# Optimization experiments

Measured on AMD Instinct MI355X. Metric: run time of the kernel, lower is better.

Reference implementation:

```python
import jax, jax.numpy as jnp
import numpy as np

H = 1024      # hidden_size
NH = 16       # num heads
HD = H // NH  # head dim


def setup_inputs() -> dict:
    key = jax.random.key(0)
    ks = jax.random.split(key, 10)
    s = 1.0 / np.sqrt(H)
    return {
        "hidden_states": jax.random.normal(ks[0], (2, 2048, H), jnp.float32),
        "attention_mask": jnp.zeros((2, 1, 1, 2048), jnp.float32),
        "Wq": jax.random.uniform(ks[1], (H, H), jnp.float32, -s, s),
        "bq": jnp.zeros((H,), jnp.float32),
        "Wk": jax.random.uniform(ks[2], (H, H), jnp.float32, -s, s),
        "bk": jnp.zeros((H,), jnp.float32),
        "Wv": jax.random.uniform(ks[3], (H, H), jnp.float32, -s, s),
        "bv": jnp.zeros((H,), jnp.float32),
        "Wo": jax.random.uniform(ks[4], (H, H), jnp.float32, -s, s),
        "bo": jnp.zeros((H,), jnp.float32),
    }


def _split_heads(x):
    b, s, _ = x.shape
    return x.reshape(b, s, NH, HD).transpose(0, 2, 1, 3)  # [B,NH,S,HD]


def reference(hidden_states, attention_mask, Wq, bq, Wk, bk, Wv, bv, Wo, bo):
    q = _split_heads(hidden_states @ Wq.T + bq)
    k = _split_heads(hidden_states @ Wk.T + bk)
    v = _split_heads(hidden_states @ Wv.T + bv)
    scores = jnp.einsum("bhqd,bhkd->bhqk", q, k) / np.sqrt(HD)
    scores = scores + attention_mask
    probs = jax.nn.softmax(scores, axis=-1)  # dropout prob=0 / eval mode -> no-op
    ctx = jnp.einsum("bhqk,bhkd->bhqd", probs, v)
    b, _, s, _ = ctx.shape
    ctx = ctx.transpose(0, 2, 1, 3).reshape(b, s, H)
    return ctx @ Wo.T + bo
```

## Files before the change

kernel.cpp:

```cpp
#include <hip/hip_runtime.h>
#include <hip/hip_bf16.h>

typedef __bf16 bf16_t;
typedef __bf16 bf16x8 __attribute__((ext_vector_type(8)));
typedef float f32x4 __attribute__((ext_vector_type(4)));
typedef float f32x16 __attribute__((ext_vector_type(16)));
typedef unsigned short u16;

#define DEVI __device__ __forceinline__
#define MFMA16x16x32(A, B, C) __builtin_amdgcn_mfma_f32_16x16x32_bf16(A, B, C, 0, 0, 0)
#define MFMA32x32x16(A, B, C) __builtin_amdgcn_mfma_f32_32x32x16_bf16(A, B, C, 0, 0, 0)

DEVI void gload_lds16(const void* g, void* l) {
  __builtin_amdgcn_global_load_lds(
      (const __attribute__((address_space(1))) void*)g,
      (__attribute__((address_space(3))) void*)l, 16, 0, 0);
}

DEVI u16 bits_of(bf16_t x) { return __builtin_bit_cast(u16, x); }

DEVI unsigned pk2(float lo, float hi) {
  return (unsigned)bits_of((bf16_t)lo) | ((unsigned)bits_of((bf16_t)hi) << 16);
}

DEVI bf16x8 mk_frag(unsigned s0, unsigned s1, unsigned s2, unsigned s3) {
  int4 t;
  t.x = (int)s0; t.y = (int)s1; t.z = (int)s2; t.w = (int)s3;
  return __builtin_bit_cast(bf16x8, t);
}

#if __has_builtin(__builtin_amdgcn_exp2f)
DEVI float exp2_fast(float x) { return __builtin_amdgcn_exp2f(x); }
#else
DEVI float exp2_fast(float x) { return __exp2f(x); }
#endif

__global__ void cvt_all(const float4* __restrict__ X,
                        const float4* __restrict__ Wq, const float4* __restrict__ Wk,
                        const float4* __restrict__ Wv, const float4* __restrict__ Wo,
                        ushort4* __restrict__ out) {
  int i = blockIdx.x * 256 + threadIdx.x;
  const float4* src;
  int off;
  if (i < 1048576) { src = X; off = i; }
  else {
    int j = i - 1048576;
    int seg = j >> 18;
    off = j & 262143;
    src = (seg == 0) ? Wq : (seg == 1) ? Wk : (seg == 2) ? Wv : Wo;
  }
  float4 v = src[off];
  ushort4 o;
  o.x = bits_of((bf16_t)v.x);
  o.y = bits_of((bf16_t)v.y);
  o.z = bits_of((bf16_t)v.z);
  o.w = bits_of((bf16_t)v.w);
  out[i] = o;
}

__global__ __launch_bounds__(256, 3) void gemm_bt(
    const bf16_t* __restrict__ A,
    const bf16_t* __restrict__ W0, const bf16_t* __restrict__ W1, const bf16_t* __restrict__ W2,
    const float* __restrict__ b0, const float* __restrict__ b1, const float* __restrict__ b2,
    bf16_t* o0, bf16_t* o1, bf16_t* o2, float s0, float s1, float s2) {
  constexpr int K = 1024, N = 1024;
  const int z = blockIdx.z;
  const bf16_t* W = (z == 0) ? W0 : ((z == 1) ? W1 : W2);
  const float* bias = (z == 0) ? b0 : ((z == 1) ? b1 : b2);
  bf16_t* out = (z == 0) ? o0 : ((z == 1) ? o1 : o2);
  const float scale = (z == 0) ? s0 : ((z == 1) ? s1 : s2);

  __shared__ bf16_t As[128 * 32];
  __shared__ bf16_t Bs[128 * 32];

  const int tid = threadIdx.x;
  const int wave = tid >> 6, lane = tid & 63;
  const int g = lane >> 4, l15 = lane & 15;
  const long m0 = (long)blockIdx.x * 128;
  const long n0 = (long)blockIdx.y * 128;

  const int srow = lane >> 2;
  const int scol = (lane & 3) * 8;

  const int wr = (wave >> 1) * 64;
  const int wc = (wave & 1) * 64;

  f32x4 acc[4][4] = {};

  for (int k0 = 0; k0 < K; k0 += 32) {
    __syncthreads();
#pragma unroll
    for (int t = 0; t < 2; ++t) {
      int chunk = wave * 2 + t;
      int row = chunk * 16 + srow;
      gload_lds16(A + (m0 + row) * K + k0 + scol, (char*)As + chunk * 1024);
      gload_lds16(W + (n0 + row) * K + k0 + scol, (char*)Bs + chunk * 1024);
    }
    __syncthreads();

    bf16x8 af[4], bfr[4];
#pragma unroll
    for (int i = 0; i < 4; ++i)
      af[i] = *(const bf16x8*)(As + (wr + i * 16 + l15) * 32 + g * 8);
#pragma unroll
    for (int i = 0; i < 4; ++i)
      bfr[i] = *(const bf16x8*)(Bs + (wc + i * 16 + l15) * 32 + g * 8);
    __builtin_amdgcn_s_setprio(1);
#pragma unroll
    for (int mi = 0; mi < 4; ++mi)
#pragma unroll
      for (int ni = 0; ni < 4; ++ni)
        acc[mi][ni] = MFMA16x16x32(af[mi], bfr[ni], acc[mi][ni]);
    __builtin_amdgcn_s_setprio(0);
  }

#pragma unroll
  for (int ni = 0; ni < 4; ++ni) {
    long col = n0 + wc + ni * 16 + l15;
    float bv = bias[col];
#pragma unroll
    for (int mi = 0; mi < 4; ++mi) {
#pragma unroll
      for (int r = 0; r < 4; ++r) {
        long row = m0 + wr + mi * 16 + g * 4 + r;
        out[row * N + col] = (bf16_t)((acc[mi][ni][r] + bv) * scale);
      }
    }
  }
}

__global__ __launch_bounds__(256, 3) void gemm_o64(
    const bf16_t* __restrict__ A, const bf16_t* __restrict__ W,
    const float* __restrict__ bias, float* __restrict__ out) {
  constexpr int K = 1024, N = 1024;
  __shared__ bf16_t As[128 * 32];
  __shared__ bf16_t Bs[64 * 32];

  const int tid = threadIdx.x;
  const int wave = tid >> 6, lane = tid & 63;
  const int g = lane >> 4, l15 = lane & 15;
  const long m0 = (long)blockIdx.x * 128;
  const long n0 = (long)blockIdx.y * 64;

  const int srow = lane >> 2;
  const int scol = (lane & 3) * 8;

  const int wr = (wave >> 1) * 64;
  const int wc = (wave & 1) * 32;

  f32x4 acc[4][2] = {};

  for (int k0 = 0; k0 < K; k0 += 32) {
    __syncthreads();
#pragma unroll
    for (int c = 0; c < 3; ++c) {
      int idx = wave * 3 + c;
      if (idx < 8) {
        int row = idx * 16 + srow;
        gload_lds16(A + (m0 + row) * K + k0 + scol, (char*)As + idx * 1024);
      } else {
        int row = (idx - 8) * 16 + srow;
        gload_lds16(W + (n0 + row) * K + k0 + scol, (char*)Bs + (idx - 8) * 1024);
      }
    }
    __syncthreads();

    bf16x8 af[4], bfr[2];
#pragma unroll
    for (int i = 0; i < 4; ++i)
      af[i] = *(const bf16x8*)(As + (wr + i * 16 + l15) * 32 + g * 8);
#pragma unroll
    for (int i = 0; i < 2; ++i)
      bfr[i] = *(const bf16x8*)(Bs + (wc + i * 16 + l15) * 32 + g * 8);
    __builtin_amdgcn_s_setprio(1);
#pragma unroll
    for (int mi = 0; mi < 4; ++mi)
#pragma unroll
      for (int ni = 0; ni < 2; ++ni)
        acc[mi][ni] = MFMA16x16x32(af[mi], bfr[ni], acc[mi][ni]);
    __builtin_amdgcn_s_setprio(0);
  }

#pragma unroll
  for (int ni = 0; ni < 2; ++ni) {
    long col = n0 + wc + ni * 16 + l15;
    float bv = bias[col];
#pragma unroll
    for (int mi = 0; mi < 4; ++mi) {
#pragma unroll
      for (int r = 0; r < 4; ++r) {
        long row = m0 + wr + mi * 16 + g * 4 + r;
        out[row * N + col] = acc[mi][ni][r] + bv;
      }
    }
  }
}

__global__ __launch_bounds__(256, 2) void attn_fwd10(
    const bf16_t* __restrict__ Qm, const bf16_t* __restrict__ Km,
    const bf16_t* __restrict__ Vm, const float* __restrict__ mask,
    bf16_t* __restrict__ ctx) {
  constexpr int S = 2048, Hs = 1024;
  constexpr float L2E = 1.4426950408889634f;
  int id = blockIdx.y * 16 + blockIdx.x;
  int swz = ((id & 7) << 6) | (id >> 3);
  const int qb = swz & 15;
  const int bh = swz >> 4;
  const int b = bh >> 4, h = bh & 15;

  const int tid = threadIdx.x;
  const int wave = tid >> 6, lane = tid & 63;
  const int l31 = lane & 31, hi = lane >> 5;

  __shared__ bf16_t Kb_[2][64 * 64];
  __shared__ bf16_t Vb_[2][64 * 64];
  __shared__ float Ms[2048];

  const char* Kg = (const char*)(Km + ((long)b * S) * Hs + h * 64);
  const bf16_t* Vg = Vm + ((long)b * S) * Hs + h * 64;
  const float* mrow = mask + b * S;

  const long qrow = (long)b * S + qb * 128 + wave * 32 + l31;
  const bf16_t* Qr = Qm + qrow * Hs + h * 64 + hi * 8;
  bf16x8 qB[4];
#pragma unroll
  for (int ks = 0; ks < 4; ++ks) qB[ks] = *(const bf16x8*)(Qr + ks * 16);

  const int ka = tid & 15, dq = tid >> 4;
  const bf16_t* Vsrc0 = Vg + (long)(4 * ka) * Hs + dq * 4;

  const int krow_in8 = lane >> 3;
  const int kslot = (lane & 7) ^ krow_in8;

#pragma unroll
  for (int c = 0; c < 2; ++c) {
    int ch = wave * 2 + c;
    gload_lds16((const char*)mrow + ch * 1024 + lane * 16, (char*)Ms + ch * 1024);
  }
#pragma unroll
  for (int c = 0; c < 2; ++c) {
    int ch = wave * 2 + c;
    gload_lds16(Kg + (long)(ch * 8 + krow_in8) * (Hs * 2) + kslot * 16,
                (char*)Kb_[0] + ch * 1024);
  }
  int2 v0 = *(const int2*)(Vsrc0);
  int2 v1 = *(const int2*)(Vsrc0 + Hs);
  int2 v2 = *(const int2*)(Vsrc0 + 2 * Hs);
  int2 v3 = *(const int2*)(Vsrc0 + 3 * Hs);
  {
    const u16* p0 = (const u16*)&v0; const u16* p1 = (const u16*)&v1;
    const u16* p2 = (const u16*)&v2; const u16* p3 = (const u16*)&v3;
#pragma unroll
    for (int j = 0; j < 4; ++j) {
      int d = dq * 4 + j;
      int2 w;
      w.x = (int)((unsigned)p0[j] | ((unsigned)p1[j] << 16));
      w.y = (int)((unsigned)p2[j] | ((unsigned)p3[j] << 16));
      *(int2*)((char*)Vb_[0] + d * 128 + ((8 * ka) ^ ((d & 7) << 4))) = w;
    }
  }
  __syncthreads();

  f32x16 acc0 = {}, acc1 = {};
  float rho = 0.0f, lrun = 0.0f;
  bf16x8 pbP[4] = {};
  bf16x8 vaP[8] = {};

  for (int t = 0; t < 32; ++t) {
    const int cur = t & 1;
    const char* kb_c = (const char*)Kb_[cur];
    const char* vb_c = (const char*)Vb_[cur];

    bf16x8 kf0[4], kf1[4];
#pragma unroll
    for (int ks = 0; ks < 4; ++ks)
      kf0[ks] = *(const bf16x8*)(kb_c + l31 * 128 + (((2 * ks + hi) * 16) ^ ((l31 & 7) << 4)));
#pragma unroll
    for (int ks = 0; ks < 4; ++ks) {
      int row = 32 + l31;
      kf1[ks] = *(const bf16x8*)(kb_c + row * 128 + (((2 * ks + hi) * 16) ^ ((row & 7) << 4)));
    }

    if (t < 31) {
      const bf16_t* Vs = Vsrc0 + (long)((t + 1) * 64) * Hs;
      v0 = *(const int2*)(Vs);
      v1 = *(const int2*)(Vs + Hs);
      v2 = *(const int2*)(Vs + 2 * Hs);
      v3 = *(const int2*)(Vs + 3 * Hs);
#pragma unroll
      for (int c = 0; c < 2; ++c) {
        int ch = wave * 2 + c;
        gload_lds16(Kg + (long)((t + 1) * 64 + ch * 8 + krow_in8) * (Hs * 2) + kslot * 16,
                    (char*)Kb_[cur ^ 1] + ch * 1024);
      }
    }
    const float* mbase = Ms + t * 64;
    float4 mk[8];
#pragma unroll
    for (int st = 0; st < 2; ++st)
#pragma unroll
      for (int rg = 0; rg < 4; ++rg)
        mk[st * 4 + rg] = *(const float4*)(mbase + st * 32 + rg * 8 + hi * 4);

    f32x16 sc0 = {}, sc1 = {};
    __builtin_amdgcn_s_setprio(1);
#pragma unroll
    for (int ks = 0; ks < 4; ++ks) sc0 = MFMA32x32x16(kf0[ks], qB[ks], sc0);
#pragma unroll
    for (int ks = 0; ks < 4; ++ks) sc1 = MFMA32x32x16(kf1[ks], qB[ks], sc1);
    __builtin_amdgcn_s_setprio(0);

    if (t > 0) {
      __builtin_amdgcn_s_setprio(1);
#pragma unroll
      for (int st = 0; st < 2; ++st)
#pragma unroll
        for (int ks2 = 0; ks2 < 2; ++ks2) {
          int i = st * 2 + ks2;
          acc0 = MFMA32x32x16(vaP[i * 2 + 0], pbP[i], acc0);
          acc1 = MFMA32x32x16(vaP[i * 2 + 1], pbP[i], acc1);
        }
      __builtin_amdgcn_s_setprio(0);
    }

#pragma unroll
    for (int st = 0; st < 2; ++st)
#pragma unroll
      for (int ks2 = 0; ks2 < 2; ++ks2) {
        int slot = st * 4 + ks2 * 2 + hi;
        int i = st * 2 + ks2;
        vaP[i * 2 + 0] = *(const bf16x8*)(vb_c + l31 * 128 + ((slot * 16) ^ ((l31 & 7) << 4)));
        int d1 = 32 + l31;
        vaP[i * 2 + 1] = *(const bf16x8*)(vb_c + d1 * 128 + ((slot * 16) ^ ((d1 & 7) << 4)));
      }

    float m4[4] = {-1e30f, -1e30f, -1e30f, -1e30f};
#pragma unroll
    for (int st = 0; st < 2; ++st) {
      f32x16& s = st ? sc1 : sc0;
#pragma unroll
      for (int rg = 0; rg < 4; ++rg) {
        float4 m = mk[st * 4 + rg];
#pragma unroll
        for (int i = 0; i < 4; ++i) {
          float v = fmaf(((const float*)&m)[i], L2E, s[rg * 4 + i]);
          s[rg * 4 + i] = v;
          m4[i] = fmaxf(m4[i], v);
        }
      }
    }
    float mt = fmaxf(fmaxf(m4[0], m4[1]), fmaxf(m4[2], m4[3]));
    mt = fmaxf(mt, __shfl_xor(mt, 32, 64));

    if (!__all(mt - rho <= 24.0f)) {
      float mw = mt;
#pragma unroll
      for (int off = 1; off < 32; off <<= 1) mw = fmaxf(mw, __shfl_xor(mw, off, 64));
      float fct = exp2_fast(rho - mw);
      lrun *= fct;
#pragma unroll
      for (int i = 0; i < 16; ++i) { acc0[i] *= fct; acc1[i] *= fct; }
      rho = mw;
    }
    float rho_u = __builtin_amdgcn_readfirstlane(rho);
    if (rho_u != 0.0f) {
#pragma unroll
      for (int i = 0; i < 16; ++i) { sc0[i] -= rho_u; sc1[i] -= rho_u; }
    }

    float s4[4] = {0.f, 0.f, 0.f, 0.f};
#pragma unroll
    for (int st = 0; st < 2; ++st) {
      f32x16& s = st ? sc1 : sc0;
#pragma unroll
      for (int i = 0; i < 16; ++i) {
        float p = exp2_fast(s[i]);
        s[i] = p;
        s4[i & 3] += p;
      }
    }
    float ls = (s4[0] + s4[1]) + (s4[2] + s4[3]);
    ls += __shfl_xor(ls, 32, 64);
    lrun += ls;

#pragma unroll
    for (int st = 0; st < 2; ++st) {
      f32x16& s = st ? sc1 : sc0;
      unsigned a0 = pk2(s[0], s[1]),   b0 = pk2(s[4], s[5]);
      unsigned a1 = pk2(s[2], s[3]),   b1 = pk2(s[6], s[7]);
      unsigned a2 = pk2(s[8], s[9]),   b2 = pk2(s[12], s[13]);
      unsigned a3 = pk2(s[10], s[11]), b3 = pk2(s[14], s[15]);
      asm("v_permlane32_swap_b32 %0, %1" : "+v"(a0), "+v"(b0));
      asm("v_permlane32_swap_b32 %0, %1" : "+v"(a1), "+v"(b1));
      asm("v_permlane32_swap_b32 %0, %1" : "+v"(a2), "+v"(b2));
      asm("v_permlane32_swap_b32 %0, %1" : "+v"(a3), "+v"(b3));
      pbP[st * 2 + 0] = mk_frag(a0, a1, b0, b1);
      pbP[st * 2 + 1] = mk_frag(a2, a3, b2, b3);
    }

    if (t < 31) {
      const u16* p0 = (const u16*)&v0; const u16* p1 = (const u16*)&v1;
      const u16* p2 = (const u16*)&v2; const u16* p3 = (const u16*)&v3;
      char* vb_n = (char*)Vb_[cur ^ 1];
#pragma unroll
      for (int j = 0; j < 4; ++j) {
        int d = dq * 4 + j;
        int2 w;
        w.x = (int)((unsigned)p0[j] | ((unsigned)p1[j] << 16));
        w.y = (int)((unsigned)p2[j] | ((unsigned)p3[j] << 16));
        *(int2*)(vb_n + d * 128 + ((8 * ka) ^ ((d & 7) << 4))) = w;
      }
    }
    __syncthreads();
  }

  __builtin_amdgcn_s_setprio(1);
#pragma unroll
  for (int st = 0; st < 2; ++st)
#pragma unroll
    for (int ks2 = 0; ks2 < 2; ++ks2) {
      int i = st * 2 + ks2;
      acc0 = MFMA32x32x16(vaP[i * 2 + 0], pbP[i], acc0);
      acc1 = MFMA32x32x16(vaP[i * 2 + 1], pbP[i], acc1);
    }
  __builtin_amdgcn_s_setprio(0);

  float inv = 1.0f / lrun;
  bf16_t* cb = ctx + qrow * Hs + h * 64;
#pragma unroll
  for (int dh = 0; dh < 2; ++dh) {
    f32x16& a = dh ? acc1 : acc0;
#pragma unroll
    for (int rg = 0; rg < 4; ++rg) {
      ushort4 o;
      o.x = bits_of((bf16_t)(a[rg * 4 + 0] * inv));
      o.y = bits_of((bf16_t)(a[rg * 4 + 1] * inv));
      o.z = bits_of((bf16_t)(a[rg * 4 + 2] * inv));
      o.w = bits_of((bf16_t)(a[rg * 4 + 3] * inv));
      *(ushort4*)(cb + dh * 32 + rg * 8 + hi * 4) = o;
    }
  }
}

extern "C" void kernel_launch(void* const* d_in, const int* in_sizes, int n_in,
                              void* d_out, int out_size, void* d_ws, size_t ws_size,
                              hipStream_t stream) {
  (void)in_sizes; (void)n_in; (void)out_size; (void)ws_size;
  const float* X  = (const float*)d_in[0];
  const float* mask = (const float*)d_in[1];
  const float* Wq = (const float*)d_in[2];
  const float* bq = (const float*)d_in[3];
  const float* Wk = (const float*)d_in[4];
  const float* bk = (const float*)d_in[5];
  const float* Wv = (const float*)d_in[6];
  const float* bv = (const float*)d_in[7];
  const float* Wo = (const float*)d_in[8];
  const float* bo = (const float*)d_in[9];

  char* ws = (char*)d_ws;
  bf16_t* Xb  = (bf16_t*)(ws + 0);
  bf16_t* Wqb = (bf16_t*)(ws + 8388608);
  bf16_t* Wkb = (bf16_t*)(ws + 10485760);
  bf16_t* Wvb = (bf16_t*)(ws + 12582912);
  bf16_t* Wob = (bf16_t*)(ws + 14680064);
  bf16_t* Qb  = (bf16_t*)(ws + 16777216);
  bf16_t* Kb  = (bf16_t*)(ws + 25165824);
  bf16_t* Vb  = (bf16_t*)(ws + 33554432);
  bf16_t* Cb  = (bf16_t*)(ws + 41943040);

  cvt_all<<<8192, 256, 0, stream>>>((const float4*)X, (const float4*)Wq, (const float4*)Wk,
                                    (const float4*)Wv, (const float4*)Wo, (ushort4*)Xb);

  const float QSCALE = 0.125f * 1.4426950408889634f;
  dim3 gq(32, 8, 3);
  gemm_bt<<<gq, 256, 0, stream>>>(Xb, Wqb, Wkb, Wvb, bq, bk, bv, Qb, Kb, Vb,
                                  QSCALE, 1.0f, 1.0f);

  dim3 ga(16, 32, 1);
  attn_fwd10<<<ga, 256, 0, stream>>>(Qb, Kb, Vb, mask, Cb);

  dim3 go(32, 16, 1);
  gemm_o64<<<go, 256, 0, stream>>>(Cb, Wob, bo, (float*)d_out);
}
```

Measured before the change: 125.7 us.

## Double attention block to 512 threads covering 256 queries per K/V tile

The attention kernel now launches 512 threads (8 waves) per block, with each block handling 256 query rows instead of 128, and the grid halves. Each K/V tile loaded into LDS is reused by twice as many queries, and the cooperative K, mask and V staging is spread over more threads, so each thread does fewer loads. The trade-off is fewer blocks, larger blocks with a heavier __syncthreads, and V stores narrowed to 4-byte writes that may raise LDS store cost.

```diff
diff --git a/kernel.cpp b/kernel.cpp
--- a/kernel.cpp
+++ b/kernel.cpp
@@ -196,16 +196,16 @@
   }
 }
 
-__global__ __launch_bounds__(256, 2) void attn_fwd10(
+__global__ __launch_bounds__(512, 2) void attn_fwd11(
     const bf16_t* __restrict__ Qm, const bf16_t* __restrict__ Km,
     const bf16_t* __restrict__ Vm, const float* __restrict__ mask,
     bf16_t* __restrict__ ctx) {
   constexpr int S = 2048, Hs = 1024;
   constexpr float L2E = 1.4426950408889634f;
-  int id = blockIdx.y * 16 + blockIdx.x;
-  int swz = ((id & 7) << 6) | (id >> 3);
-  const int qb = swz & 15;
-  const int bh = swz >> 4;
+  int id = blockIdx.y * 8 + blockIdx.x;
+  int swz = ((id & 7) << 5) | (id >> 3);
+  const int qb = swz & 7;
+  const int bh = swz >> 3;
   const int b = bh >> 4, h = bh & 15;
 
   const int tid = threadIdx.x;
@@ -220,43 +220,30 @@
   const bf16_t* Vg = Vm + ((long)b * S) * Hs + h * 64;
   const float* mrow = mask + b * S;
 
-  const long qrow = (long)b * S + qb * 128 + wave * 32 + l31;
+  const long qrow = (long)b * S + qb * 256 + wave * 32 + l31;
   const bf16_t* Qr = Qm + qrow * Hs + h * 64 + hi * 8;
   bf16x8 qB[4];
 #pragma unroll
   for (int ks = 0; ks < 4; ++ks) qB[ks] = *(const bf16x8*)(Qr + ks * 16);
 
-  const int ka = tid & 15, dq = tid >> 4;
-  const bf16_t* Vsrc0 = Vg + (long)(4 * ka) * Hs + dq * 4;
+  const int ka2 = tid & 31, dq = tid >> 5;
+  const bf16_t* Vsrc0 = Vg + (long)(2 * ka2) * Hs + dq * 4;
 
   const int krow_in8 = lane >> 3;
   const int kslot = (lane & 7) ^ krow_in8;
 
-#pragma unroll
-  for (int c = 0; c < 2; ++c) {
-    int ch = wave * 2 + c;
-    gload_lds16((const char*)mrow + ch * 1024 + lane * 16, (char*)Ms + ch * 1024);
-  }
-#pragma unroll
-  for (int c = 0; c < 2; ++c) {
-    int ch = wave * 2 + c;
-    gload_lds16(Kg + (long)(ch * 8 + krow_in8) * (Hs * 2) + kslot * 16,
-                (char*)Kb_[0] + ch * 1024);
-  }
+  gload_lds16((const char*)mrow + wave * 1024 + lane * 16, (char*)Ms + wave * 1024);
+  gload_lds16(Kg + (long)(wave * 8 + krow_in8) * (Hs * 2) + kslot * 16,
+              (char*)Kb_[0] + wave * 1024);
   int2 v0 = *(const int2*)(Vsrc0);
   int2 v1 = *(const int2*)(Vsrc0 + Hs);
-  int2 v2 = *(const int2*)(Vsrc0 + 2 * Hs);
-  int2 v3 = *(const int2*)(Vsrc0 + 3 * Hs);
   {
     const u16* p0 = (const u16*)&v0; const u16* p1 = (const u16*)&v1;
-    const u16* p2 = (const u16*)&v2; const u16* p3 = (const u16*)&v3;
 #pragma unroll
     for (int j = 0; j < 4; ++j) {
       int d = dq * 4 + j;
-      int2 w;
-      w.x = (int)((unsigned)p0[j] | ((unsigned)p1[j] << 16));
-      w.y = (int)((unsigned)p2[j] | ((unsigned)p3[j] << 16));
-      *(int2*)((char*)Vb_[0] + d * 128 + ((8 * ka) ^ ((d & 7) << 4))) = w;
+      int w = (int)((unsigned)p0[j] | ((unsigned)p1[j] << 16));
+      *(int*)((char*)Vb_[0] + d * 128 + ((4 * ka2) ^ ((d & 7) << 4))) = w;
     }
   }
   __syncthreads();
@@ -285,14 +272,8 @@
       const bf16_t* Vs = Vsrc0 + (long)((t + 1) * 64) * Hs;
       v0 = *(const int2*)(Vs);
       v1 = *(const int2*)(Vs + Hs);
-      v2 = *(const int2*)(Vs + 2 * Hs);
-      v3 = *(const int2*)(Vs + 3 * Hs);
-#pragma unroll
-      for (int c = 0; c < 2; ++c) {
-        int ch = wave * 2 + c;
-        gload_lds16(Kg + (long)((t + 1) * 64 + ch * 8 + krow_in8) * (Hs * 2) + kslot * 16,
-                    (char*)Kb_[cur ^ 1] + ch * 1024);
-      }
+      gload_lds16(Kg + (long)((t + 1) * 64 + wave * 8 + krow_in8) * (Hs * 2) + kslot * 16,
+                  (char*)Kb_[cur ^ 1] + wave * 1024);
     }
     const float* mbase = Ms + t * 64;
     float4 mk[8];
@@ -400,15 +381,12 @@
 
     if (t < 31) {
       const u16* p0 = (const u16*)&v0; const u16* p1 = (const u16*)&v1;
-      const u16* p2 = (const u16*)&v2; const u16* p3 = (const u16*)&v3;
       char* vb_n = (char*)Vb_[cur ^ 1];
 #pragma unroll
       for (int j = 0; j < 4; ++j) {
         int d = dq * 4 + j;
-        int2 w;
-        w.x = (int)((unsigned)p0[j] | ((unsigned)p1[j] << 16));
-        w.y = (int)((unsigned)p2[j] | ((unsigned)p3[j] << 16));
-        *(int2*)(vb_n + d * 128 + ((8 * ka) ^ ((d & 7) << 4))) = w;
+        int w = (int)((unsigned)p0[j] | ((unsigned)p1[j] << 16));
+        *(int*)(vb_n + d * 128 + ((4 * ka2) ^ ((d & 7) << 4))) = w;
       }
     }
     __syncthreads();
@@ -476,8 +454,8 @@
   gemm_bt<<<gq, 256, 0, stream>>>(Xb, Wqb, Wkb, Wvb, bq, bk, bv, Qb, Kb, Vb,
                                   QSCALE, 1.0f, 1.0f);
 
-  dim3 ga(16, 32, 1);
-  attn_fwd10<<<ga, 256, 0, stream>>>(Qb, Kb, Vb, mask, Cb);
+  dim3 ga(8, 32, 1);
+  attn_fwd11<<<ga, 512, 0, stream>>>(Qb, Kb, Vb, mask, Cb);
 
   dim3 go(32, 16, 1);
   gemm_o64<<<go, 256, 0, stream>>>(Cb, Wob, bo, (float*)d_out);
```

Result: faster. 122.6 us, median of 4 (-2.5%).

## Double attention block size to 256 queries and 128-key tiles with 8 waves

Applied to the files above, without the earlier changes.

The attention kernel now runs 512 threads (8 waves) per block covering 256 query rows, and iterates over 128-key tiles (16 iterations instead of 32). Each K/V tile loaded to LDS is shared by twice as many queries, and there are half as many barriers and loop iterations. In exchange, LDS per block roughly doubles, per-thread register pressure rises (four score accumulators, larger P/V fragment arrays), and the grid shrinks to 256 blocks, which may reduce occupancy or fill on the GPU's compute units. The mask is now read from LDS inline instead of being prefetched into registers.

```diff
diff --git a/kernel.cpp b/kernel.cpp
--- a/kernel.cpp
+++ b/kernel.cpp
@@ -196,47 +196,43 @@
   }
 }
 
-__global__ __launch_bounds__(256, 2) void attn_fwd10(
+__global__ __launch_bounds__(512, 2) void attn_fwd13(
     const bf16_t* __restrict__ Qm, const bf16_t* __restrict__ Km,
     const bf16_t* __restrict__ Vm, const float* __restrict__ mask,
     bf16_t* __restrict__ ctx) {
   constexpr int S = 2048, Hs = 1024;
   constexpr float L2E = 1.4426950408889634f;
-  int id = blockIdx.y * 16 + blockIdx.x;
-  int swz = ((id & 7) << 6) | (id >> 3);
-  const int qb = swz & 15;
-  const int bh = swz >> 4;
+  int id = blockIdx.y * 8 + blockIdx.x;
+  int swz = ((id & 7) << 5) | (id >> 3);
+  const int qb = swz & 7;
+  const int bh = swz >> 3;
   const int b = bh >> 4, h = bh & 15;
 
   const int tid = threadIdx.x;
   const int wave = tid >> 6, lane = tid & 63;
   const int l31 = lane & 31, hi = lane >> 5;
 
-  __shared__ bf16_t Kb_[2][64 * 64];
-  __shared__ bf16_t Vb_[2][64 * 64];
+  __shared__ bf16_t Kb_[2][128 * 64];
+  __shared__ bf16_t Vb_[2][64 * 128];
   __shared__ float Ms[2048];
 
   const char* Kg = (const char*)(Km + ((long)b * S) * Hs + h * 64);
   const bf16_t* Vg = Vm + ((long)b * S) * Hs + h * 64;
   const float* mrow = mask + b * S;
 
-  const long qrow = (long)b * S + qb * 128 + wave * 32 + l31;
+  const long qrow = (long)b * S + qb * 256 + wave * 32 + l31;
   const bf16_t* Qr = Qm + qrow * Hs + h * 64 + hi * 8;
   bf16x8 qB[4];
 #pragma unroll
   for (int ks = 0; ks < 4; ++ks) qB[ks] = *(const bf16x8*)(Qr + ks * 16);
 
-  const int ka = tid & 15, dq = tid >> 4;
-  const bf16_t* Vsrc0 = Vg + (long)(4 * ka) * Hs + dq * 4;
+  const int ka2 = tid & 31, dq = tid >> 5;
+  const bf16_t* Vsrc0 = Vg + (long)(4 * ka2) * Hs + dq * 4;
 
   const int krow_in8 = lane >> 3;
   const int kslot = (lane & 7) ^ krow_in8;
 
-#pragma unroll
-  for (int c = 0; c < 2; ++c) {
-    int ch = wave * 2 + c;
-    gload_lds16((const char*)mrow + ch * 1024 + lane * 16, (char*)Ms + ch * 1024);
-  }
+  gload_lds16((const char*)mrow + wave * 1024 + lane * 16, (char*)Ms + wave * 1024);
 #pragma unroll
   for (int c = 0; c < 2; ++c) {
     int ch = wave * 2 + c;
@@ -256,33 +252,23 @@
       int2 w;
       w.x = (int)((unsigned)p0[j] | ((unsigned)p1[j] << 16));
       w.y = (int)((unsigned)p2[j] | ((unsigned)p3[j] << 16));
-      *(int2*)((char*)Vb_[0] + d * 128 + ((8 * ka) ^ ((d & 7) << 4))) = w;
+      *(int2*)((char*)Vb_[0] + d * 256 + ((8 * ka2) ^ ((d & 7) << 4))) = w;
     }
   }
   __syncthreads();
 
   f32x16 acc0 = {}, acc1 = {};
   float rho = 0.0f, lrun = 0.0f;
-  bf16x8 pbP[4] = {};
-  bf16x8 vaP[8] = {};
-
-  for (int t = 0; t < 32; ++t) {
+  bf16x8 pbP[8] = {};
+  bf16x8 vaP[16] = {};
+
+  for (int t = 0; t < 16; ++t) {
     const int cur = t & 1;
     const char* kb_c = (const char*)Kb_[cur];
     const char* vb_c = (const char*)Vb_[cur];
 
-    bf16x8 kf0[4], kf1[4];
-#pragma unroll
-    for (int ks = 0; ks < 4; ++ks)
-      kf0[ks] = *(const bf16x8*)(kb_c + l31 * 128 + (((2 * ks + hi) * 16) ^ ((l31 & 7) << 4)));
-#pragma unroll
-    for (int ks = 0; ks < 4; ++ks) {
-      int row = 32 + l31;
-      kf1[ks] = *(const bf16x8*)(kb_c + row * 128 + (((2 * ks + hi) * 16) ^ ((row & 7) << 4)));
-    }
-
-    if (t < 31) {
-      const bf16_t* Vs = Vsrc0 + (long)((t + 1) * 64) * Hs;
+    if (t < 15) {
+      const bf16_t* Vs = Vsrc0 + (long)((t + 1) * 128) * Hs;
       v0 = *(const int2*)(Vs);
       v1 = *(const int2*)(Vs + Hs);
       v2 = *(const int2*)(Vs + 2 * Hs);
@@ -290,57 +276,53 @@
 #pragma unroll
       for (int c = 0; c < 2; ++c) {
         int ch = wave * 2 + c;
-        gload_lds16(Kg + (long)((t + 1) * 64 + ch * 8 + krow_in8) * (Hs * 2) + kslot * 16,
+        gload_lds16(Kg + (long)((t + 1) * 128 + ch * 8 + krow_in8) * (Hs * 2) + kslot * 16,
                     (char*)Kb_[cur ^ 1] + ch * 1024);
       }
     }
-    const float* mbase = Ms + t * 64;
-    float4 mk[8];
-#pragma unroll
-    for (int st = 0; st < 2; ++st)
-#pragma unroll
-      for (int rg = 0; rg < 4; ++rg)
-        mk[st * 4 + rg] = *(const float4*)(mbase + st * 32 + rg * 8 + hi * 4);
-
-    f32x16 sc0 = {}, sc1 = {};
+
+    f32x16 sc0 = {}, sc1 = {}, sc2 = {}, sc3 = {};
     __builtin_amdgcn_s_setprio(1);
 #pragma unroll
-    for (int ks = 0; ks < 4; ++ks) sc0 = MFMA32x32x16(kf0[ks], qB[ks], sc0);
-#pragma unroll
-    for (int ks = 0; ks < 4; ++ks) sc1 = MFMA32x32x16(kf1[ks], qB[ks], sc1);
+    for (int st = 0; st < 4; ++st) {
+      f32x16& s = (st == 0) ? sc0 : (st == 1) ? sc1 : (st == 2) ? sc2 : sc3;
+      int row = st * 32 + l31;
+      int sw = (row & 7) << 4;
+      bf16x8 kf[4];
+#pragma unroll
+      for (int ks = 0; ks < 4; ++ks)
+        kf[ks] = *(const bf16x8*)(kb_c + row * 128 + (((2 * ks + hi) * 16) ^ sw));
+#pragma unroll
+      for (int ks = 0; ks < 4; ++ks) s = MFMA32x32x16(kf[ks], qB[ks], s);
+    }
     __builtin_amdgcn_s_setprio(0);
 
     if (t > 0) {
       __builtin_amdgcn_s_setprio(1);
 #pragma unroll
-      for (int st = 0; st < 2; ++st)
-#pragma unroll
-        for (int ks2 = 0; ks2 < 2; ++ks2) {
-          int i = st * 2 + ks2;
-          acc0 = MFMA32x32x16(vaP[i * 2 + 0], pbP[i], acc0);
-          acc1 = MFMA32x32x16(vaP[i * 2 + 1], pbP[i], acc1);
-        }
+      for (int i5 = 0; i5 < 8; ++i5) {
+        acc0 = MFMA32x32x16(vaP[i5 * 2 + 0], pbP[i5], acc0);
+        acc1 = MFMA32x32x16(vaP[i5 * 2 + 1], pbP[i5], acc1);
+      }
       __builtin_amdgcn_s_setprio(0);
     }
 
 #pragma unroll
-    for (int st = 0; st < 2; ++st)
-#pragma unroll
-      for (int ks2 = 0; ks2 < 2; ++ks2) {
-        int slot = st * 4 + ks2 * 2 + hi;
-        int i = st * 2 + ks2;
-        vaP[i * 2 + 0] = *(const bf16x8*)(vb_c + l31 * 128 + ((slot * 16) ^ ((l31 & 7) << 4)));
-        int d1 = 32 + l31;
-        vaP[i * 2 + 1] = *(const bf16x8*)(vb_c + d1 * 128 + ((slot * 16) ^ ((d1 & 7) << 4)));
-      }
-
+    for (int i5 = 0; i5 < 8; ++i5) {
+      int slot = i5 * 2 + hi;
+      int d0 = l31, d1 = 32 + l31;
+      vaP[i5 * 2 + 0] = *(const bf16x8*)(vb_c + d0 * 256 + ((slot * 16) ^ ((d0 & 7) << 4)));
+      vaP[i5 * 2 + 1] = *(const bf16x8*)(vb_c + d1 * 256 + ((slot * 16) ^ ((d1 & 7) << 4)));
+    }
+
+    const float* mbase = Ms + t * 128;
     float m4[4] = {-1e30f, -1e30f, -1e30f, -1e30f};
 #pragma unroll
-    for (int st = 0; st < 2; ++st) {
-      f32x16& s = st ? sc1 : sc0;
+    for (int st = 0; st < 4; ++st) {
+      f32x16& s = (st == 0) ? sc0 : (st == 1) ? sc1 : (st == 2) ? sc2 : sc3;
 #pragma unroll
       for (int rg = 0; rg < 4; ++rg) {
-        float4 m = mk[st * 4 + rg];
+        float4 m = *(const float4*)(mbase + st * 32 + rg * 8 + hi * 4);
 #pragma unroll
         for (int i = 0; i < 4; ++i) {
           float v = fmaf(((const float*)&m)[i], L2E, s[rg * 4 + i]);
@@ -365,13 +347,15 @@
     float rho_u = __builtin_amdgcn_readfirstlane(rho);
     if (rho_u != 0.0f) {
 #pragma unroll
-      for (int i = 0; i < 16; ++i) { sc0[i] -= rho_u; sc1[i] -= rho_u; }
+      for (int i = 0; i < 16; ++i) {
+        sc0[i] -= rho_u; sc1[i] -= rho_u; sc2[i] -= rho_u; sc3[i] -= rho_u;
+      }
     }
 
     float s4[4] = {0.f, 0.f, 0.f, 0.f};
 #pragma unroll
-    for (int st = 0; st < 2; ++st) {
-      f32x16& s = st ? sc1 : sc0;
+    for (int st = 0; st < 4; ++st) {
+      f32x16& s = (st == 0) ? sc0 : (st == 1) ? sc1 : (st == 2) ? sc2 : sc3;
 #pragma unroll
       for (int i = 0; i < 16; ++i) {
         float p = exp2_fast(s[i]);
@@ -384,8 +368,8 @@
     lrun += ls;
 
 #pragma unroll
-    for (int st = 0; st < 2; ++st) {
-      f32x16& s = st ? sc1 : sc0;
+    for (int st = 0; st < 4; ++st) {
+      f32x16& s = (st == 0) ? sc0 : (st == 1) ? sc1 : (st == 2) ? sc2 : sc3;
       unsigned a0 = pk2(s[0], s[1]),   b0 = pk2(s[4], s[5]);
       unsigned a1 = pk2(s[2], s[3]),   b1 = pk2(s[6], s[7]);
       unsigned a2 = pk2(s[8], s[9]),   b2 = pk2(s[12], s[13]);
@@ -398,7 +382,7 @@
       pbP[st * 2 + 1] = mk_frag(a2, a3, b2, b3);
     }
 
-    if (t < 31) {
+    if (t < 15) {
       const u16* p0 = (const u16*)&v0; const u16* p1 = (const u16*)&v1;
       const u16* p2 = (const u16*)&v2; const u16* p3 = (const u16*)&v3;
       char* vb_n = (char*)Vb_[cur ^ 1];
@@ -408,7 +392,7 @@
         int2 w;
         w.x = (int)((unsigned)p0[j] | ((unsigned)p1[j] << 16));
         w.y = (int)((unsigned)p2[j] | ((unsigned)p3[j] << 16));
-        *(int2*)(vb_n + d * 128 + ((8 * ka) ^ ((d & 7) << 4))) = w;
+        *(int2*)(vb_n + d * 256 + ((8 * ka2) ^ ((d & 7) << 4))) = w;
       }
     }
     __syncthreads();
@@ -416,13 +400,10 @@
 
   __builtin_amdgcn_s_setprio(1);
 #pragma unroll
-  for (int st = 0; st < 2; ++st)
-#pragma unroll
-    for (int ks2 = 0; ks2 < 2; ++ks2) {
-      int i = st * 2 + ks2;
-      acc0 = MFMA32x32x16(vaP[i * 2 + 0], pbP[i], acc0);
-      acc1 = MFMA32x32x16(vaP[i * 2 + 1], pbP[i], acc1);
-    }
+  for (int i5 = 0; i5 < 8; ++i5) {
+    acc0 = MFMA32x32x16(vaP[i5 * 2 + 0], pbP[i5], acc0);
+    acc1 = MFMA32x32x16(vaP[i5 * 2 + 1], pbP[i5], acc1);
+  }
   __builtin_amdgcn_s_setprio(0);
 
   float inv = 1.0f / lrun;
@@ -476,8 +457,8 @@
   gemm_bt<<<gq, 256, 0, stream>>>(Xb, Wqb, Wkb, Wvb, bq, bk, bv, Qb, Kb, Vb,
                                   QSCALE, 1.0f, 1.0f);
 
-  dim3 ga(16, 32, 1);
-  attn_fwd10<<<ga, 256, 0, stream>>>(Qb, Kb, Vb, mask, Cb);
+  dim3 ga(8, 32, 1);
+  attn_fwd13<<<ga, 512, 0, stream>>>(Qb, Kb, Vb, mask, Cb);
 
   dim3 go(32, 16, 1);
   gemm_o64<<<go, 256, 0, stream>>>(Cb, Wob, bo, (float*)d_out);
```

Measured after the change: 153.9 us. 1.22x slower.
